# Performance work log

Measured on AMD Instinct MI355X. Metric: run time of the kernel, lower is better.

## Reference

```python
import jax, jax.numpy as jnp
import numpy as np

B, S, DM = 2, 2048, 1024
H, HD = 16, 64  # heads, head_dims = dims // heads
SCALE = HD ** -0.5


def softmax_one(x):
    # softmax with +1 in the denominator: exp(x_i) / (1 + sum_j exp(x_j))
    # stable form: shift by m = max(max(x), 0)
    m = jnp.maximum(jnp.max(x, axis=-1, keepdims=True), 0.0)
    e = jnp.exp(x - m)
    return e / (jnp.exp(-m) + jnp.sum(e, axis=-1, keepdims=True))


def setup_inputs() -> dict:
    key = jax.random.key(0)
    ks = jax.random.split(key, 11)
    init = lambda k, shape, fan_in: jax.random.uniform(k, shape, jnp.float32, -1.0, 1.0) * (fan_in ** -0.5)
    return {
        "query": jax.random.normal(ks[0], (B, S, DM), jnp.float32),
        "key": jax.random.normal(ks[1], (B, S, DM), jnp.float32),
        "value": jax.random.normal(ks[2], (B, S, DM), jnp.float32),
        "Wq": init(ks[3], (H * HD, DM), DM), "bq": init(ks[4], (H * HD,), DM),
        "Wk": init(ks[5], (H * HD, DM), DM), "bk": init(ks[6], (H * HD,), DM),
        "Wv": init(ks[7], (H * HD, DM), DM), "bv": init(ks[8], (H * HD,), DM),
        "Wo": init(ks[9], (DM, H * HD), H * HD), "bo": init(ks[10], (DM,), H * HD),
    }


def _proj(x, W, b):
    # [B,S,DM] -> [B,H,S,HD]
    y = x @ W.T + b
    return y.reshape(B, S, H, HD).transpose(0, 2, 1, 3)


def reference(query, key, value, Wq, bq, Wk, bk, Wv, bv, Wo, bo):
    Q = _proj(query, Wq, bq)
    K = _proj(key, Wk, bk)
    V = _proj(value, Wv, bv)
    scores = jnp.einsum("bhqd,bhkd->bhqk", Q, K) * SCALE  # [B,H,S,S]
    attn = softmax_one(scores)
    out = jnp.einsum("bhqk,bhkd->bhqd", attn, V)  # [B,H,S,HD]
    out = out.transpose(0, 2, 1, 3).reshape(B, S, H * HD)
    return out @ Wo.T + bo
```

## Files before the change

### kernel.cpp

```cpp
#include <hip/hip_runtime.h>

#define B_ 2
#define S_ 2048
#define DM_ 1024
#define H_ 16
#define HD_ 64
#define QSCALE_ 0.18033688011112042f

typedef __bf16 bf16;
typedef _Float16 f16;
typedef __attribute__((ext_vector_type(4))) __bf16 bf16x4;
typedef __attribute__((ext_vector_type(8))) __bf16 bf16x8;
typedef __attribute__((ext_vector_type(8))) _Float16 f16x8;
typedef __attribute__((ext_vector_type(4))) float f32x4;

#define MFMA16(a, b, c) __builtin_amdgcn_mfma_f32_16x16x32_bf16((a), (b), (c), 0, 0, 0)
#define EXP2(x) __builtin_amdgcn_exp2f(x)

__device__ __forceinline__ void async16(const bf16* g, bf16* l) {
  __builtin_amdgcn_global_load_lds(
      (const __attribute__((address_space(1))) void*)g,
      (__attribute__((address_space(3))) void*)l, 16, 0, 0);
}

__global__ __launch_bounds__(256) void convert_kernel(
    const float* __restrict__ q, const float* __restrict__ k,
    const float* __restrict__ v, const float* __restrict__ wq,
    const float* __restrict__ wk, const float* __restrict__ wv,
    const float* __restrict__ wo, bf16* __restrict__ dst) {
  size_t idx = ((size_t)blockIdx.x * 256 + threadIdx.x) * 8;
  const float* src;
  size_t off;
  if (idx < 4194304) { src = q; off = idx; }
  else if (idx < 8388608) { src = k; off = idx - 4194304; }
  else if (idx < 12582912) { src = v; off = idx - 8388608; }
  else if (idx < 13631488) { src = wq; off = idx - 12582912; }
  else if (idx < 14680064) { src = wk; off = idx - 13631488; }
  else if (idx < 15728640) { src = wv; off = idx - 14680064; }
  else { src = wo; off = idx - 15728640; }
  float4 a = *(const float4*)(src + off);
  float4 b = *(const float4*)(src + off + 4);
  bf16x8 o;
  o[0] = (bf16)a.x; o[1] = (bf16)a.y; o[2] = (bf16)a.z; o[3] = (bf16)a.w;
  o[4] = (bf16)b.x; o[5] = (bf16)b.y; o[6] = (bf16)b.z; o[7] = (bf16)b.w;
  *(bf16x8*)(dst + idx) = o;
}

template <int MODE>
__device__ __forceinline__ void gemm_body(const bf16* A, const bf16* W,
                                          const float* bias, bf16* C,
                                          float scale) {
  constexpr int K = 1024;
  __shared__ __align__(16) bf16 smem[128 * 136];
  bf16* As = smem;
  bf16* Bs = smem + 128 * 64;
  const int t = threadIdx.x;
  const int lane = t & 63, wave = t >> 6;
  const int quad = lane >> 4, l16 = lane & 15;
  const int m0 = blockIdx.y * 128, n0 = blockIdx.x * 128;
  const int wm = (wave >> 1) * 64, wn = (wave & 1) * 64;

  const f32x4 zero = {0.f, 0.f, 0.f, 0.f};
  f32x4 acc[4][4];
  for (int i = 0; i < 4; i++)
    for (int j = 0; j < 4; j++) acc[i][j] = zero;

  for (int k0 = 0; k0 < K; k0 += 64) {
    for (int i = 0; i < 4; ++i) {
      int c = i * 256 + t;
      int row = c >> 3, g = c & 7;
      int off = k0 + ((g ^ (row & 7)) * 8);
      async16(A + (size_t)(m0 + row) * K + off, As + c * 8);
      async16(W + (size_t)(n0 + row) * K + off, Bs + c * 8);
    }
    __syncthreads();

    for (int ks = 0; ks < 2; ks++) {
      bf16x8 af[4], bfr[4];
      for (int mb = 0; mb < 4; mb++) {
        int ra = wm + mb * 16 + l16;
        af[mb] = *(const bf16x8*)(As + ra * 64 + ((ks * 4 + quad) ^ (ra & 7)) * 8);
        int rb = wn + mb * 16 + l16;
        bfr[mb] = *(const bf16x8*)(Bs + rb * 64 + ((ks * 4 + quad) ^ (rb & 7)) * 8);
      }
      for (int mb = 0; mb < 4; mb++)
        for (int nb = 0; nb < 4; nb++)
          acc[mb][nb] = MFMA16(af[mb], bfr[nb], acc[mb][nb]);
    }
    __syncthreads();
  }

  if constexpr (MODE == 2) {
    bf16* Ct = smem;
    for (int nb = 0; nb < 4; nb++) {
      int cl = wn + nb * 16 + l16;
      float bv = bias[n0 + cl] * scale;
      for (int mb = 0; mb < 4; mb++) {
        int rowb = wm + mb * 16 + quad * 4;
        bf16x4 v;
        for (int r = 0; r < 4; r++)
          v[r] = (bf16)(acc[mb][nb][r] * scale + bv);
        *(bf16x4*)(Ct + cl * 136 + rowb) = v;
      }
    }
    __syncthreads();
    int c = t >> 1, half = t & 1;
    int colg = n0 + c;
    int hh = colg >> 6, dd = colg & 63;
    int bb = m0 >> 11, s0 = m0 & (S_ - 1);
    bf16* dst = C + (((size_t)(bb * H_ + hh)) * HD_ + dd) * S_ + s0 + half * 64;
    const bf16* srcr = Ct + c * 136 + half * 64;
    for (int j = 0; j < 8; ++j)
      *(bf16x8*)(dst + j * 8) = *(const bf16x8*)(srcr + j * 8);
  } else {
    for (int nb = 0; nb < 4; nb++) {
      int col = n0 + wn + nb * 16 + l16;
      float bv = bias[col] * scale;
      for (int mb = 0; mb < 4; mb++) {
        int rowb = m0 + wm + mb * 16 + quad * 4;
        for (int r = 0; r < 4; r++) {
          int row = rowb + r;
          float o = acc[mb][nb][r] * scale + bv;
          int bb = row >> 11, s = row & (S_ - 1);
          int h = col >> 6, d = col & 63;
          C[(((size_t)(bb * H_ + h)) * S_ + s) * HD_ + d] = (bf16)o;
        }
      }
    }
  }
}

__global__ __launch_bounds__(256, 4) void qkv_proj_kernel(
    const bf16* Xc, const float* bq, const float* bk, const float* bv,
    bf16* Qo, bf16* Ko, bf16* Vo) {
  int z = blockIdx.z;
  const bf16* A = Xc + (size_t)z * 4194304;
  const bf16* W = Xc + 12582912 + (size_t)z * 1048576;
  if (z == 0)
    gemm_body<1>(A, W, bq, Qo, QSCALE_);
  else if (z == 1)
    gemm_body<1>(A, W, bk, Ko, 1.0f);
  else
    gemm_body<2>(A, W, bv, Vo, 1.0f);
}

__global__ __launch_bounds__(256, 4) void out_proj_kernel(const bf16* A,
                                                          const bf16* W,
                                                          const float* bias,
                                                          float* C) {
  constexpr int K = 1024, N = 1024;
  __shared__ __align__(16) bf16 As[64 * 64];
  __shared__ __align__(16) bf16 Bs[64 * 64];
  const int t = threadIdx.x;
  const int lane = t & 63, wave = t >> 6;
  const int quad = lane >> 4, l16 = lane & 15;
  const int m0 = blockIdx.y * 64, n0 = blockIdx.x * 64;

  const f32x4 zero = {0.f, 0.f, 0.f, 0.f};
  f32x4 acc[4];
  for (int i = 0; i < 4; i++) acc[i] = zero;

  for (int k0 = 0; k0 < K; k0 += 64) {
    for (int i = 0; i < 2; ++i) {
      int c = i * 256 + t;
      int row = c >> 3, g = c & 7;
      int off = k0 + ((g ^ (row & 7)) * 8);
      async16(A + (size_t)(m0 + row) * K + off, As + c * 8);
      async16(W + (size_t)(n0 + row) * K + off, Bs + c * 8);
    }
    __syncthreads();

    for (int ks = 0; ks < 2; ks++) {
      int ra = wave * 16 + l16;
      bf16x8 af = *(const bf16x8*)(As + ra * 64 + ((ks * 4 + quad) ^ (ra & 7)) * 8);
      for (int nb = 0; nb < 4; nb++) {
        int rb = nb * 16 + l16;
        bf16x8 bfr =
            *(const bf16x8*)(Bs + rb * 64 + ((ks * 4 + quad) ^ (rb & 7)) * 8);
        acc[nb] = MFMA16(af, bfr, acc[nb]);
      }
    }
    __syncthreads();
  }

  for (int nb = 0; nb < 4; nb++) {
    int col = n0 + nb * 16 + l16;
    float bv = bias[col];
    int rowb = m0 + wave * 16 + quad * 4;
    for (int r = 0; r < 4; r++)
      C[(size_t)(rowb + r) * N + col] = acc[nb][r] + bv;
  }
}

__global__ __launch_bounds__(256) void attn_kernel(
    const bf16* __restrict__ Q, const bf16* __restrict__ Kg,
    const bf16* __restrict__ VTg, f16* __restrict__ Pa0,
    f16* __restrict__ Pa1, float* __restrict__ rsA0,
    float* __restrict__ rsA1) {
  __shared__ __align__(16) bf16 Ks[128 * 64];
  __shared__ __align__(16) bf16 Vt[64 * 128];
  __shared__ __align__(16) bf16 Ps[4 * 16 * 136];
  const int t = threadIdx.x;
  const int lane = t & 63, wave = t >> 6;
  const int quad = lane >> 4, l16 = lane & 15;
  const int id = blockIdx.x;
  const int bh = id & 31;
  const int rest = id >> 5;
  const int split = rest & 1;
  const int q0 = (rest >> 1) * 128;
  const int b = bh >> 4, h = bh & 15;
  const size_t base = ((size_t)(b * H_ + h)) * S_ * HD_;
  const bf16* Qp = Q + base;
  const bf16* Kp = Kg + base;
  const bf16* Vp = VTg + base;
  f16* Pa = split ? Pa1 : Pa0;
  float* rsA = split ? rsA1 : rsA0;

  bf16x8 aq[2][2];
  for (int s = 0; s < 2; s++) {
    const bf16* qr = Qp + (size_t)(q0 + wave * 32 + s * 16 + l16) * HD_;
    aq[s][0] = *(const bf16x8*)(qr + quad * 8);
    aq[s][1] = *(const bf16x8*)(qr + 32 + quad * 8);
  }

  const f32x4 zero = {0.f, 0.f, 0.f, 0.f};
  f32x4 oc[2][4];
  for (int s = 0; s < 2; s++)
    for (int d = 0; d < 4; d++) oc[s][d] = zero;
  float rs[2] = {0.f, 0.f};

  bf16* Pw = Ps + wave * (16 * 136);
  const int kvbeg = split * 1024;

  for (int kv0 = kvbeg; kv0 < kvbeg + 1024; kv0 += 128) {
    for (int i = 0; i < 4; ++i) {
      int c = i * 256 + t;
      int row = c >> 3, g = c & 7;
      async16(Kp + (size_t)(kv0 + row) * HD_ + (g ^ (row & 7)) * 8, Ks + c * 8);
    }
    for (int i = 0; i < 4; ++i) {
      int c = i * 256 + t;
      int d = c >> 4, g = c & 15;
      async16(Vp + (size_t)d * S_ + kv0 + (g ^ (d & 15)) * 8, Vt + c * 8);
    }
    __syncthreads();

    f32x4 sc[2][8];
    for (int s = 0; s < 2; s++)
      for (int nb = 0; nb < 8; nb++) sc[s][nb] = zero;
    for (int ks = 0; ks < 2; ks++) {
      for (int nb = 0; nb < 8; nb++) {
        int row = nb * 16 + l16;
        int slot = (ks * 4 + quad) ^ (row & 7);
        bf16x8 kf = *(const bf16x8*)(Ks + row * 64 + slot * 8);
        sc[0][nb] = MFMA16(kf, aq[0][ks], sc[0][nb]);
        sc[1][nb] = MFMA16(kf, aq[1][ks], sc[1][nb]);
      }
    }

    for (int s = 0; s < 2; s++) {
      bf16* prow = Pw + l16 * 136 + quad * 4;
      for (int nb = 0; nb < 8; nb++) {
        float p0 = EXP2(sc[s][nb][0]);
        float p1 = EXP2(sc[s][nb][1]);
        float p2 = EXP2(sc[s][nb][2]);
        float p3 = EXP2(sc[s][nb][3]);
        rs[s] += (p0 + p1) + (p2 + p3);
        bf16x4 pv = {(bf16)p0, (bf16)p1, (bf16)p2, (bf16)p3};
        *(bf16x4*)(prow + nb * 16) = pv;
      }
      for (int ks = 0; ks < 4; ks++) {
        bf16x8 ap = *(const bf16x8*)(Pw + l16 * 136 + ks * 32 + quad * 8);
        for (int db = 0; db < 4; db++) {
          int row = db * 16 + l16;
          int slot = (ks * 4 + quad) ^ (row & 15);
          bf16x8 vf = *(const bf16x8*)(Vt + row * 128 + slot * 8);
          oc[s][db] = MFMA16(ap, vf, oc[s][db]);
        }
      }
    }
    __syncthreads();
  }

  for (int s = 0; s < 2; s++) {
    float rtot = rs[s];
    rtot += __shfl_xor(rtot, 16);
    rtot += __shfl_xor(rtot, 32);
    if (quad == 0)
      rsA[(size_t)(b * H_ + h) * S_ + q0 + wave * 32 + s * 16 + l16] = rtot;
    for (int r = 0; r < 4; r++) {
      int qrow = q0 + wave * 32 + s * 16 + quad * 4 + r;
      size_t orow = ((size_t)(b * S_ + qrow) * H_ + h) * HD_;
      for (int db = 0; db < 4; db++)
        Pa[orow + db * 16 + l16] = (f16)(oc[s][db][r]);
    }
  }
}

__global__ __launch_bounds__(256) void normalize_kernel(
    const f16* __restrict__ Pa0, const f16* __restrict__ Pa1,
    const float* __restrict__ rs0, const float* __restrict__ rs1,
    bf16* __restrict__ Ow) {
  size_t flat = ((size_t)blockIdx.x * 256 + threadIdx.x) * 8;
  int h = (int)((flat >> 6) & 15);
  int s = (int)((flat >> 10) & 2047);
  int b = (int)(flat >> 21);
  int ri = (b * H_ + h) * S_ + s;
  float inv = 1.f / (1.f + rs0[ri] + rs1[ri]);
  f16x8 a = *(const f16x8*)(Pa0 + flat);
  f16x8 c = *(const f16x8*)(Pa1 + flat);
  bf16x8 o;
  for (int j = 0; j < 8; j++)
    o[j] = (bf16)(((float)a[j] + (float)c[j]) * inv);
  *(bf16x8*)(Ow + flat) = o;
}

extern "C" void kernel_launch(void* const* d_in, const int* in_sizes, int n_in,
                              void* d_out, int out_size, void* d_ws,
                              size_t ws_size, hipStream_t stream) {
  const float* query = (const float*)d_in[0];
  const float* key = (const float*)d_in[1];
  const float* value = (const float*)d_in[2];
  const float* bq = (const float*)d_in[4];
  const float* bk = (const float*)d_in[6];
  const float* bv = (const float*)d_in[8];
  const float* bo = (const float*)d_in[10];
  float* out = (float*)d_out;

  bf16* Xc = (bf16*)d_ws;
  bf16* Qw = Xc + 16777216;
  const size_t SZ = (size_t)B_ * H_ * S_ * HD_;
  bf16* Kw = Qw + SZ;
  bf16* Vw = Kw + SZ;
  bf16* Ow = Vw + SZ;
  f16* Pa0 = (f16*)d_ws;
  f16* Pa1 = Pa0 + SZ;
  float* rs0 = (float*)((char*)d_ws + 16777216);
  float* rs1 = rs0 + (size_t)B_ * H_ * S_;

  convert_kernel<<<8192, 256, 0, stream>>>(query, key, value,
                                           (const float*)d_in[3],
                                           (const float*)d_in[5],
                                           (const float*)d_in[7],
                                           (const float*)d_in[9], Xc);
  qkv_proj_kernel<<<dim3(8, 32, 3), 256, 0, stream>>>(Xc, bq, bk, bv, Qw, Kw,
                                                      Vw);
  attn_kernel<<<1024, 256, 0, stream>>>(Qw, Kw, Vw, Pa0, Pa1, rs0, rs1);
  normalize_kernel<<<2048, 256, 0, stream>>>(Pa0, Pa1, rs0, rs1, Ow);
  out_proj_kernel<<<dim3(16, 64), 256, 0, stream>>>(Ow, Xc + 15728640, bo,
                                                    out);
}
```

Measured before the change: 244.8 us.

## Widen attention blocks to 8 waves and split KV three ways

The attention kernel now runs 512-thread blocks covering 256 query rows, so each K/V tile staged in LDS is shared by twice as many waves. The KV range is split into three uneven parts (640/640/768) instead of two halves, giving 768 blocks. A third partial-output buffer and row-sum array are added, and the normalize kernel sums all three. The changes are meant to cut redundant K/V global traffic and rebalance the grid, at the cost of more partial-output writes and reads, an uneven last split, and higher per-block LDS use.

```diff
diff --git a/kernel.cpp b/kernel.cpp
--- a/kernel.cpp
+++ b/kernel.cpp
@@ -192,29 +192,29 @@
   }
 }
 
-__global__ __launch_bounds__(256) void attn_kernel(
+__global__ __launch_bounds__(512) void attn_kernel(
     const bf16* __restrict__ Q, const bf16* __restrict__ Kg,
     const bf16* __restrict__ VTg, f16* __restrict__ Pa0,
-    f16* __restrict__ Pa1, float* __restrict__ rsA0,
-    float* __restrict__ rsA1) {
+    f16* __restrict__ Pa1, f16* __restrict__ Pa2, float* __restrict__ rsA0,
+    float* __restrict__ rsA1, float* __restrict__ rsA2) {
   __shared__ __align__(16) bf16 Ks[128 * 64];
   __shared__ __align__(16) bf16 Vt[64 * 128];
-  __shared__ __align__(16) bf16 Ps[4 * 16 * 136];
+  __shared__ __align__(16) bf16 Ps[8 * 16 * 136];
   const int t = threadIdx.x;
   const int lane = t & 63, wave = t >> 6;
   const int quad = lane >> 4, l16 = lane & 15;
   const int id = blockIdx.x;
   const int bh = id & 31;
   const int rest = id >> 5;
-  const int split = rest & 1;
-  const int q0 = (rest >> 1) * 128;
+  const int qt = rest / 3, split = rest % 3;
+  const int q0 = qt * 256;
   const int b = bh >> 4, h = bh & 15;
   const size_t base = ((size_t)(b * H_ + h)) * S_ * HD_;
   const bf16* Qp = Q + base;
   const bf16* Kp = Kg + base;
   const bf16* Vp = VTg + base;
-  f16* Pa = split ? Pa1 : Pa0;
-  float* rsA = split ? rsA1 : rsA0;
+  f16* Pa = split == 0 ? Pa0 : (split == 1 ? Pa1 : Pa2);
+  float* rsA = split == 0 ? rsA0 : (split == 1 ? rsA1 : rsA2);
 
   bf16x8 aq[2][2];
   for (int s = 0; s < 2; s++) {
@@ -230,16 +230,17 @@
   float rs[2] = {0.f, 0.f};
 
   bf16* Pw = Ps + wave * (16 * 136);
-  const int kvbeg = split * 1024;
-
-  for (int kv0 = kvbeg; kv0 < kvbeg + 1024; kv0 += 128) {
-    for (int i = 0; i < 4; ++i) {
-      int c = i * 256 + t;
+  const int kvbeg = split * 640;
+  const int kvend = (split == 2) ? 2048 : kvbeg + 640;
+
+  for (int kv0 = kvbeg; kv0 < kvend; kv0 += 128) {
+    for (int i = 0; i < 2; ++i) {
+      int c = i * 512 + t;
       int row = c >> 3, g = c & 7;
       async16(Kp + (size_t)(kv0 + row) * HD_ + (g ^ (row & 7)) * 8, Ks + c * 8);
     }
-    for (int i = 0; i < 4; ++i) {
-      int c = i * 256 + t;
+    for (int i = 0; i < 2; ++i) {
+      int c = i * 512 + t;
       int d = c >> 4, g = c & 15;
       async16(Vp + (size_t)d * S_ + kv0 + (g ^ (d & 15)) * 8, Vt + c * 8);
     }
@@ -299,19 +300,21 @@
 
 __global__ __launch_bounds__(256) void normalize_kernel(
     const f16* __restrict__ Pa0, const f16* __restrict__ Pa1,
-    const float* __restrict__ rs0, const float* __restrict__ rs1,
+    const f16* __restrict__ Pa2, const float* __restrict__ rs0,
+    const float* __restrict__ rs1, const float* __restrict__ rs2,
     bf16* __restrict__ Ow) {
   size_t flat = ((size_t)blockIdx.x * 256 + threadIdx.x) * 8;
   int h = (int)((flat >> 6) & 15);
   int s = (int)((flat >> 10) & 2047);
   int b = (int)(flat >> 21);
   int ri = (b * H_ + h) * S_ + s;
-  float inv = 1.f / (1.f + rs0[ri] + rs1[ri]);
+  float inv = 1.f / (1.f + rs0[ri] + rs1[ri] + rs2[ri]);
   f16x8 a = *(const f16x8*)(Pa0 + flat);
   f16x8 c = *(const f16x8*)(Pa1 + flat);
+  f16x8 e = *(const f16x8*)(Pa2 + flat);
   bf16x8 o;
   for (int j = 0; j < 8; j++)
-    o[j] = (bf16)(((float)a[j] + (float)c[j]) * inv);
+    o[j] = (bf16)(((float)a[j] + (float)c[j] + (float)e[j]) * inv);
   *(bf16x8*)(Ow + flat) = o;
 }
 
@@ -335,8 +338,10 @@
   bf16* Ow = Vw + SZ;
   f16* Pa0 = (f16*)d_ws;
   f16* Pa1 = Pa0 + SZ;
-  float* rs0 = (float*)((char*)d_ws + 16777216);
+  f16* Pa2 = Pa1 + SZ;
+  float* rs0 = (float*)((char*)d_ws + 25165824);
   float* rs1 = rs0 + (size_t)B_ * H_ * S_;
+  float* rs2 = rs1 + (size_t)B_ * H_ * S_;
 
   convert_kernel<<<8192, 256, 0, stream>>>(query, key, value,
                                            (const float*)d_in[3],
@@ -345,8 +350,9 @@
                                            (const float*)d_in[9], Xc);
   qkv_proj_kernel<<<dim3(8, 32, 3), 256, 0, stream>>>(Xc, bq, bk, bv, Qw, Kw,
                                                       Vw);
-  attn_kernel<<<1024, 256, 0, stream>>>(Qw, Kw, Vw, Pa0, Pa1, rs0, rs1);
-  normalize_kernel<<<2048, 256, 0, stream>>>(Pa0, Pa1, rs0, rs1, Ow);
+  attn_kernel<<<768, 512, 0, stream>>>(Qw, Kw, Vw, Pa0, Pa1, Pa2, rs0, rs1,
+                                       rs2);
+  normalize_kernel<<<2048, 256, 0, stream>>>(Pa0, Pa1, Pa2, rs0, rs1, rs2, Ow);
   out_proj_kernel<<<dim3(16, 64), 256, 0, stream>>>(Ow, Xc + 15728640, bo,
                                                     out);
 }
```

New measurement: 244.9 us. About the same (+0.0%).
